# Kernel optimization log

Measured on AMD Instinct MI355X. Metric: run time of the kernel, lower is better.

## Reference

```python
import jax, jax.numpy as jnp
import numpy as np
from jax import lax

B, T, E, H = 16, 1024, 512, 1024


def setup_inputs() -> dict:
    key = jax.random.key(0)
    ks = jax.random.split(key, 10)
    s = 0.1
    return {
        "x":   jax.random.normal(ks[0], (B, T, E), jnp.float32),
        # reset gate: sigmoid(x@Wxr + h@Whr + br)
        "Wxr": jax.random.normal(ks[1], (E, H), jnp.float32) * s,
        "Whr": jax.random.normal(ks[2], (H, H), jnp.float32) * s,
        "br":  jax.random.normal(ks[3], (H,), jnp.float32) * s,
        # update gate: sigmoid(x@Wxz + h@Whz + bz)
        "Wxz": jax.random.normal(ks[4], (E, H), jnp.float32) * s,
        "Whz": jax.random.normal(ks[5], (H, H), jnp.float32) * s,
        "bz":  jax.random.normal(ks[6], (H,), jnp.float32) * s,
        # candidate: tanh(r * (h@Wh) + x@Wi + b)
        "Wi":  jax.random.normal(ks[7], (E, H), jnp.float32) * s,
        "Wh":  jax.random.normal(ks[8], (H, H), jnp.float32) * s,
        "b":   jax.random.normal(ks[9], (H,), jnp.float32) * s,
    }


def reference(x, Wxr, Whr, br, Wxz, Whz, bz, Wi, Wh, b):
    # Batch all input-to-hidden projections across time up front.
    xr = jnp.einsum("bte,eh->bth", x, Wxr) + br  # [B,T,H]
    xz = jnp.einsum("bte,eh->bth", x, Wxz) + bz
    xi = jnp.einsum("bte,eh->bth", x, Wi) + b

    def step(h, inp):
        xr_t, xz_t, xi_t = inp  # each [B,H]
        r = jax.nn.sigmoid(xr_t + h @ Whr)
        z = jax.nn.sigmoid(xz_t + h @ Whz)
        cand = jnp.tanh(r * (h @ Wh) + xi_t)
        h_new = z * h + (1.0 - z) * cand
        return h_new, h_new

    h0 = jnp.zeros((x.shape[0], Wh.shape[0]), x.dtype)
    # scan over time: move T to leading axis
    _, hs = lax.scan(step, h0, (xr.transpose(1, 0, 2), xz.transpose(1, 0, 2), xi.transpose(1, 0, 2)))
    return hs.transpose(1, 0, 2)  # [B,T,H]
```

## Files before the change

kernel.cpp:

```cpp
#include <hip/hip_runtime.h>
#include <hip/hip_bf16.h>
#include <cstddef>
#include <cstdint>

static constexpr int BB = 16;
static constexpr int TT = 1024;
static constexpr int EE = 512;
static constexpr int HH = 1024;

static constexpr int NG   = 4;
static constexpr int GBLK = 64;
static constexpr int BPG  = 4;
static constexpr int COLS = 16;

using u32 = unsigned int;
typedef float f32x4 __attribute__((ext_vector_type(4)));

static constexpr u32 PZ = 0x7FC0DEADu;

__device__ __forceinline__ float st_load(const float* p) { return *p; }
__device__ __forceinline__ float st_load(const __hip_bfloat16* p) { return __bfloat162float(*p); }
__device__ __forceinline__ void st_store(float* p, float v) { *p = v; }
__device__ __forceinline__ void st_store(__hip_bfloat16* p, float v) { *p = __float2bfloat16(v); }

__device__ __forceinline__ void llc_load(f32x4& d, const f32x4* p) {
    asm volatile("global_load_dwordx4 %0, %1, off sc0 sc1" : "=v"(d) : "v"(p));
}
__device__ __forceinline__ void llc_drain() {
    asm volatile("s_waitcnt vmcnt(0)" ::: "memory");
    __builtin_amdgcn_sched_barrier(0);
}
__device__ __forceinline__ bool ok4(const f32x4 v) {
    return __float_as_uint(v[0]) != PZ && __float_as_uint(v[1]) != PZ &&
           __float_as_uint(v[2]) != PZ && __float_as_uint(v[3]) != PZ;
}

#define FMA4(ACC, S, W)                         \
    (ACC).x = fmaf((S), (W).x, (ACC).x);        \
    (ACC).y = fmaf((S), (W).y, (ACC).y);        \
    (ACC).z = fmaf((S), (W).z, (ACC).z);        \
    (ACC).w = fmaf((S), (W).w, (ACC).w);

template <typename ST>
__global__ __launch_bounds__(256) void proj_kernel(
    const float* __restrict__ x,
    const float* __restrict__ Wxr, const float* __restrict__ br,
    const float* __restrict__ Wxz, const float* __restrict__ bz,
    const float* __restrict__ Wi,  const float* __restrict__ bi,
    ST* __restrict__ xr_out, ST* __restrict__ xz_out, float* __restrict__ xi_out,
    u32* __restrict__ bar)
{
    __shared__ float xT[16][68];
    __shared__ float wB[3][16][64];

    const int tid = threadIdx.x;
    if (blockIdx.x == 0 && blockIdx.y == 0) bar[tid] = 0u;

    const int tx = tid & 15, ty = tid >> 4;
    const int m0 = blockIdx.y * 64, n0 = blockIdx.x * 64;
    const float* Wg[3] = {Wxr, Wxz, Wi};

    float4 acc[3][4];
#pragma unroll
    for (int g = 0; g < 3; ++g)
#pragma unroll
        for (int i = 0; i < 4; ++i) acc[g][i] = make_float4(0.f, 0.f, 0.f, 0.f);

    const int xrow = tid >> 2, xk = (tid & 3) * 4;
    const int wk = tid >> 4, wn = (tid & 15) * 4;

    for (int k0 = 0; k0 < EE; k0 += 16) {
        float4 xv = *(const float4*)(x + (size_t)(m0 + xrow) * EE + k0 + xk);
        xT[xk + 0][xrow] = xv.x;
        xT[xk + 1][xrow] = xv.y;
        xT[xk + 2][xrow] = xv.z;
        xT[xk + 3][xrow] = xv.w;
#pragma unroll
        for (int g = 0; g < 3; ++g) {
            float4 wv = *(const float4*)(Wg[g] + (size_t)(k0 + wk) * HH + n0 + wn);
            *(float4*)&wB[g][wk][wn] = wv;
        }
        __syncthreads();
#pragma unroll
        for (int kk = 0; kk < 16; ++kk) {
            float4 a  = *(const float4*)&xT[kk][ty * 4];
            float4 w0 = *(const float4*)&wB[0][kk][tx * 4];
            float4 w1 = *(const float4*)&wB[1][kk][tx * 4];
            float4 w2 = *(const float4*)&wB[2][kk][tx * 4];
            float as[4] = {a.x, a.y, a.z, a.w};
#pragma unroll
            for (int i = 0; i < 4; ++i) {
                FMA4(acc[0][i], as[i], w0);
                FMA4(acc[1][i], as[i], w1);
                FMA4(acc[2][i], as[i], w2);
            }
        }
        __syncthreads();
    }

    float4 bv0 = *(const float4*)(br + n0 + tx * 4);
    float4 bv1 = *(const float4*)(bz + n0 + tx * 4);
    float4 bv2 = *(const float4*)(bi + n0 + tx * 4);
#pragma unroll
    for (int i = 0; i < 4; ++i) {
        size_t m = (size_t)m0 + ty * 4 + i;
        size_t off = m * HH + n0 + tx * 4;
        float4 v0 = acc[0][i]; v0.x += bv0.x; v0.y += bv0.y; v0.z += bv0.z; v0.w += bv0.w;
        float4 v1 = acc[1][i]; v1.x += bv1.x; v1.y += bv1.y; v1.z += bv1.z; v1.w += bv1.w;
        float4 v2 = acc[2][i]; v2.x += bv2.x; v2.y += bv2.y; v2.z += bv2.z; v2.w += bv2.w;
        st_store(xr_out + off + 0, v0.x); st_store(xr_out + off + 1, v0.y);
        st_store(xr_out + off + 2, v0.z); st_store(xr_out + off + 3, v0.w);
        st_store(xz_out + off + 0, v1.x); st_store(xz_out + off + 1, v1.y);
        st_store(xz_out + off + 2, v1.z); st_store(xz_out + off + 3, v1.w);
        *(float4*)(xi_out + off) = v2;
    }
}

__device__ __forceinline__ float row16_allreduce(float v) {
    int y;
    y = __builtin_amdgcn_update_dpp(0, __float_as_int(v), 0xB1, 0xF, 0xF, true);
    v += __int_as_float(y);
    y = __builtin_amdgcn_update_dpp(0, __float_as_int(v), 0x4E, 0xF, 0xF, true);
    v += __int_as_float(y);
    y = __builtin_amdgcn_update_dpp(0, __float_as_int(v), 0x124, 0xF, 0xF, true);
    v += __int_as_float(y);
    y = __builtin_amdgcn_update_dpp(0, __float_as_int(v), 0x128, 0xF, 0xF, true);
    v += __int_as_float(y);
    return v;
}

__device__ __forceinline__ void xbar(u32* ctr, unsigned target) {
    __syncthreads();
    if (threadIdx.x == 0) {
        asm volatile("s_waitcnt vmcnt(0)" ::: "memory");
        __builtin_amdgcn_sched_barrier(0);
        __hip_atomic_fetch_add(ctr, 1u, __ATOMIC_RELAXED, __HIP_MEMORY_SCOPE_AGENT);
        while (__hip_atomic_load(ctr, __ATOMIC_RELAXED, __HIP_MEMORY_SCOPE_AGENT) < target) {
            __builtin_amdgcn_s_sleep(1);
        }
        __builtin_amdgcn_sched_barrier(0);
    }
    __syncthreads();
}

template <typename ST>
__global__ __launch_bounds__(512, 1) void scan_kernel(
    const ST* __restrict__ xr, const ST* __restrict__ xz,
    const float* __restrict__ Whr, const float* __restrict__ Whz, const float* __restrict__ Wh,
    float* __restrict__ out,
    float* __restrict__ hbuf,
    u32* __restrict__ bar)
{
    __shared__ f32x4 hsx[8][4][32];
    __shared__ float red[8][4][48];
    __shared__ float pre[48][4];

    const int tid = threadIdx.x, bid = blockIdx.x;
    const int lane = tid & 63, wv = tid >> 6;
    const int cgg = lane >> 4, kslo = lane & 15;
    const int ks = wv * 16 + kslo;
    const int group = bid >> 6, gb = bid & 63;
    const int n0 = gb * COLS;
    u32* ctr = bar + group * 64;

    float wreg[12][8];
    {
        const float* WG[3] = {Whr, Whz, Wh};
#pragma unroll
        for (int u = 0; u < 12; ++u) {
            int ugc = cgg * 12 + u;
            const float* W = WG[ugc >> 4];
            int col = n0 + (ugc & 15);
#pragma unroll
            for (int j = 0; j < 8; ++j)
                wreg[u][j] = W[(size_t)(ks * 8 + j) * HH + col];
        }
    }

    const float pzf = __uint_as_float(PZ);
    const int tb4 = tid >> 4, tc = tid & 15;
    const int tbg = group * BPG + tb4;
    const int coln = n0 + tc;

    float pxr = 0.f, pxz = 0.f, pxi = 0.f, hprev = 0.f;
    if (tid < 64) {
        float* b0 = hbuf + group * (BPG * HH) + tb4 * HH + coln;
        __hip_atomic_store(b0,         0.f, __ATOMIC_RELAXED, __HIP_MEMORY_SCOPE_AGENT);
        __hip_atomic_store(b0 + 16384, pzf, __ATOMIC_RELAXED, __HIP_MEMORY_SCOPE_AGENT);
        __hip_atomic_store(b0 + 32768, pzf, __ATOMIC_RELAXED, __HIP_MEMORY_SCOPE_AGENT);
        __hip_atomic_store(b0 + 49152, pzf, __ATOMIC_RELAXED, __HIP_MEMORY_SCOPE_AGENT);
        size_t idx0 = (size_t)(tbg * TT) * HH + coln;
        pxr = st_load(xr + idx0); pxz = st_load(xz + idx0); pxi = out[idx0];
    }
    xbar(ctr, GBLK);

    const int b_ld = lane >> 4;
    const int s_rot = (((lane & 15) + (gb & 15)) * 2) & 31;

    for (int t = 0; t < TT; ++t) {
        {
            const f32x4* p = (const f32x4*)hbuf + (size_t)(t & 3) * 4096
                             + group * 1024 + b_ld * 256 + wv * 32 + s_rot;
            f32x4 va, vb;
            for (;;) {
                llc_load(va, p); llc_load(vb, p + 1); llc_drain();
                if (ok4(va) && ok4(vb)) break;
                __builtin_amdgcn_s_sleep(1);
            }
            hsx[wv][b_ld][s_rot]     = va;
            hsx[wv][b_ld][s_rot + 1] = vb;
            asm volatile("s_waitcnt lgkmcnt(0)" ::: "memory");
            __builtin_amdgcn_sched_barrier(0);
        }

        if (tid < 64 && t + 2 < TT) {
            __hip_atomic_store(hbuf + (size_t)((t + 2) & 3) * 16384
                               + group * (BPG * HH) + tb4 * HH + coln,
                               pzf, __ATOMIC_RELAXED, __HIP_MEMORY_SCOPE_AGENT);
        }

        float pacc[4][12];
#pragma unroll
        for (int b = 0; b < 4; ++b)
#pragma unroll
            for (int u = 0; u < 12; ++u) pacc[b][u] = 0.f;

#pragma unroll
        for (int b = 0; b < 4; ++b) {
            f32x4 ha = hsx[wv][b][2 * kslo];
            f32x4 hb = hsx[wv][b][2 * kslo + 1];
#pragma unroll
            for (int u = 0; u < 12; ++u) {
                float a = pacc[b][u];
                a = fmaf(ha[0], wreg[u][0], a);
                a = fmaf(ha[1], wreg[u][1], a);
                a = fmaf(ha[2], wreg[u][2], a);
                a = fmaf(ha[3], wreg[u][3], a);
                a = fmaf(hb[0], wreg[u][4], a);
                a = fmaf(hb[1], wreg[u][5], a);
                a = fmaf(hb[2], wreg[u][6], a);
                a = fmaf(hb[3], wreg[u][7], a);
                pacc[b][u] = a;
            }
        }

#pragma unroll
        for (int b = 0; b < 4; ++b)
#pragma unroll
            for (int u = 0; u < 12; ++u) pacc[b][u] = row16_allreduce(pacc[b][u]);

        if (kslo == 0) {
#pragma unroll
            for (int b = 0; b < 4; ++b)
#pragma unroll
                for (int u = 0; u < 12; ++u) red[wv][cgg][b * 12 + u] = pacc[b][u];
        }
        __syncthreads();

        if (tid < 192) {
            int b4 = tid & 3, ugc = tid >> 2;
            int cq = ugc / 12, u = ugc - cq * 12;
            float s = 0.f;
#pragma unroll
            for (int w = 0; w < 8; ++w) s += red[w][cq][b4 * 12 + u];
            pre[ugc][b4] = s;
        }
        __syncthreads();

        if (tid < 64) {
            float dr = pre[tc][tb4], dz = pre[16 + tc][tb4], dh = pre[32 + tc][tb4];
            float r = 1.f / (1.f + expf(-(dr + pxr)));
            float z = 1.f / (1.f + expf(-(dz + pxz)));
            float cand = tanhf(fmaf(r, dh, pxi));
            float hnew = fmaf(z, hprev - cand, cand);
            hprev = hnew;
            asm volatile("s_waitcnt vmcnt(0)" ::: "memory");
            __builtin_amdgcn_sched_barrier(0);
            if (t + 1 < TT) {
                __hip_atomic_store(hbuf + (size_t)((t + 1) & 3) * 16384
                                   + group * (BPG * HH) + tb4 * HH + coln,
                                   hnew, __ATOMIC_RELAXED, __HIP_MEMORY_SCOPE_AGENT);
            }
            size_t idx = (size_t)(tbg * TT + t) * HH + coln;
            out[idx] = hnew;
            if (t + 1 < TT) {
                size_t idx2 = idx + HH;
                pxr = st_load(xr + idx2); pxz = st_load(xz + idx2); pxi = out[idx2];
            }
        }
    }
}

__global__ void sentinel_kernel(float* out) {
    if (threadIdx.x == 0 && blockIdx.x == 0) out[0] = 12345.0f;
}

extern "C" void kernel_launch(void* const* d_in, const int* in_sizes, int n_in,
                              void* d_out, int out_size, void* d_ws, size_t ws_size,
                              hipStream_t stream) {
    const float* x   = (const float*)d_in[0];
    const float* Wxr = (const float*)d_in[1];
    const float* Whr = (const float*)d_in[2];
    const float* br  = (const float*)d_in[3];
    const float* Wxz = (const float*)d_in[4];
    const float* Whz = (const float*)d_in[5];
    const float* bz  = (const float*)d_in[6];
    const float* Wi  = (const float*)d_in[7];
    const float* Wh  = (const float*)d_in[8];
    const float* bb  = (const float*)d_in[9];
    float* out = (float*)d_out;

    const size_t BTH = (size_t)BB * TT * HH;
    const size_t HBUF_ELTS = (size_t)4 * BB * HH;
    const size_t BAR_BYTES = 4096;
    const size_t need_f32 = 2 * BTH * sizeof(float) + HBUF_ELTS * sizeof(float) + BAR_BYTES;
    const size_t need_b16 = 2 * BTH * sizeof(__hip_bfloat16) + HBUF_ELTS * sizeof(float) + BAR_BYTES;

    dim3 pgrid(HH / 64, (BB * TT) / 64);

    if (ws_size >= need_f32) {
        float* xr = (float*)d_ws;
        float* xz = xr + BTH;
        float* hb = xz + BTH;
        u32* bar = (u32*)(hb + HBUF_ELTS);
        proj_kernel<float><<<pgrid, 256, 0, stream>>>(x, Wxr, br, Wxz, bz, Wi, bb, xr, xz, out, bar);
        const float* xrc = xr; const float* xzc = xz;
        void* args[8] = {(void*)&xrc, (void*)&xzc, (void*)&Whr, (void*)&Whz,
                         (void*)&Wh, (void*)&out, (void*)&hb, (void*)&bar};
        hipLaunchCooperativeKernel((void*)scan_kernel<float>, dim3(256), dim3(512),
                                   args, 0, stream);
    } else if (ws_size >= need_b16) {
        __hip_bfloat16* xr = (__hip_bfloat16*)d_ws;
        __hip_bfloat16* xz = xr + BTH;
        float* hb = (float*)(xz + BTH);
        u32* bar = (u32*)(hb + HBUF_ELTS);
        proj_kernel<__hip_bfloat16><<<pgrid, 256, 0, stream>>>(x, Wxr, br, Wxz, bz, Wi, bb, xr, xz, out, bar);
        const __hip_bfloat16* xrc = xr; const __hip_bfloat16* xzc = xz;
        void* args[8] = {(void*)&xrc, (void*)&xzc, (void*)&Whr, (void*)&Whz,
                         (void*)&Wh, (void*)&out, (void*)&hb, (void*)&bar};
        hipLaunchCooperativeKernel((void*)scan_kernel<__hip_bfloat16>, dim3(256), dim3(512),
                                   args, 0, stream);
    } else {
        sentinel_kernel<<<1, 64, 0, stream>>>(out);
    }
}
```

Measured before the change: 5.192 ms.

## Repartition GRU scan into eight smaller groups with 1024-thread blocks

The recurrent scan is split into 8 groups of 32 blocks, each handling 2 batch rows and 32 hidden columns, instead of 4 groups of 64 blocks handling 4 rows and 16 columns. Each block now runs 16 waves, split into two halves over the gate columns, and 8 K-slices per half. Each thread polls one f32x4 of the hidden state instead of two. The intent is to shrink the per-step cross-block barrier and hidden-state exchange to fewer participants and spread per-step work across more waves. The cost is higher register pressure: each thread still holds 96 weight registers, and `__launch_bounds__(1024, 4)` may force spills. Occupancy constraints for the cooperative launch also change.

```diff
diff --git a/kernel.cpp b/kernel.cpp
--- a/kernel.cpp
+++ b/kernel.cpp
@@ -8,10 +8,10 @@
 static constexpr int EE = 512;
 static constexpr int HH = 1024;
 
-static constexpr int NG   = 4;
-static constexpr int GBLK = 64;
-static constexpr int BPG  = 4;
-static constexpr int COLS = 16;
+static constexpr int NG   = 8;
+static constexpr int GBLK = 32;
+static constexpr int BPG  = 2;
+static constexpr int COLS = 32;
 
 using u32 = unsigned int;
 typedef float f32x4 __attribute__((ext_vector_type(4)));
@@ -144,47 +144,47 @@
 }
 
 template <typename ST>
-__global__ __launch_bounds__(512, 1) void scan_kernel(
+__global__ __launch_bounds__(1024, 4) void scan_kernel(
     const ST* __restrict__ xr, const ST* __restrict__ xz,
     const float* __restrict__ Whr, const float* __restrict__ Whz, const float* __restrict__ Wh,
     float* __restrict__ out,
     float* __restrict__ hbuf,
     u32* __restrict__ bar)
 {
-    __shared__ f32x4 hsx[8][4][32];
-    __shared__ float red[8][4][48];
-    __shared__ float pre[48][4];
+    __shared__ f32x4 hsx[16][BPG][32];
+    __shared__ float red[16][4][24];
+    __shared__ float pre[96][BPG];
 
     const int tid = threadIdx.x, bid = blockIdx.x;
     const int lane = tid & 63, wv = tid >> 6;
     const int cgg = lane >> 4, kslo = lane & 15;
-    const int ks = wv * 16 + kslo;
-    const int group = bid >> 6, gb = bid & 63;
+    const int wu = wv >> 3, wk = wv & 7;
+    const int group = bid >> 5, gb = bid & 31;
     const int n0 = gb * COLS;
-    u32* ctr = bar + group * 64;
+    u32* ctr = bar + group * 32;
 
     float wreg[12][8];
     {
         const float* WG[3] = {Whr, Whz, Wh};
 #pragma unroll
         for (int u = 0; u < 12; ++u) {
-            int ugc = cgg * 12 + u;
-            const float* W = WG[ugc >> 4];
-            int col = n0 + (ugc & 15);
+            int ugc = wu * 48 + cgg * 12 + u;
+            const float* W = WG[ugc >> 5];
+            int col = n0 + (ugc & 31);
 #pragma unroll
             for (int j = 0; j < 8; ++j)
-                wreg[u][j] = W[(size_t)(ks * 8 + j) * HH + col];
+                wreg[u][j] = W[(size_t)(wk * 128 + kslo * 8 + j) * HH + col];
         }
     }
 
     const float pzf = __uint_as_float(PZ);
-    const int tb4 = tid >> 4, tc = tid & 15;
-    const int tbg = group * BPG + tb4;
+    const int tb2 = tid >> 5, tc = tid & 31;
+    const int tbg = group * BPG + tb2;
     const int coln = n0 + tc;
 
     float pxr = 0.f, pxz = 0.f, pxi = 0.f, hprev = 0.f;
     if (tid < 64) {
-        float* b0 = hbuf + group * (BPG * HH) + tb4 * HH + coln;
+        float* b0 = hbuf + group * (BPG * HH) + tb2 * HH + coln;
         __hip_atomic_store(b0,         0.f, __ATOMIC_RELAXED, __HIP_MEMORY_SCOPE_AGENT);
         __hip_atomic_store(b0 + 16384, pzf, __ATOMIC_RELAXED, __HIP_MEMORY_SCOPE_AGENT);
         __hip_atomic_store(b0 + 32768, pzf, __ATOMIC_RELAXED, __HIP_MEMORY_SCOPE_AGENT);
@@ -194,39 +194,38 @@
     }
     xbar(ctr, GBLK);
 
-    const int b_ld = lane >> 4;
-    const int s_rot = (((lane & 15) + (gb & 15)) * 2) & 31;
+    const int b_ld = lane >> 5;
+    const int s_rot = ((lane & 31) + gb) & 31;
+    const int g_base = group * (BPG * 256) + b_ld * 256 + wk * 32 + s_rot;
 
     for (int t = 0; t < TT; ++t) {
         {
-            const f32x4* p = (const f32x4*)hbuf + (size_t)(t & 3) * 4096
-                             + group * 1024 + b_ld * 256 + wv * 32 + s_rot;
-            f32x4 va, vb;
+            const f32x4* p = (const f32x4*)hbuf + (size_t)(t & 3) * 4096 + g_base;
+            f32x4 va;
             for (;;) {
-                llc_load(va, p); llc_load(vb, p + 1); llc_drain();
-                if (ok4(va) && ok4(vb)) break;
+                llc_load(va, p); llc_drain();
+                if (ok4(va)) break;
                 __builtin_amdgcn_s_sleep(1);
             }
-            hsx[wv][b_ld][s_rot]     = va;
-            hsx[wv][b_ld][s_rot + 1] = vb;
+            hsx[wv][b_ld][s_rot] = va;
             asm volatile("s_waitcnt lgkmcnt(0)" ::: "memory");
             __builtin_amdgcn_sched_barrier(0);
         }
 
         if (tid < 64 && t + 2 < TT) {
             __hip_atomic_store(hbuf + (size_t)((t + 2) & 3) * 16384
-                               + group * (BPG * HH) + tb4 * HH + coln,
+                               + group * (BPG * HH) + tb2 * HH + coln,
                                pzf, __ATOMIC_RELAXED, __HIP_MEMORY_SCOPE_AGENT);
         }
 
-        float pacc[4][12];
-#pragma unroll
-        for (int b = 0; b < 4; ++b)
+        float pacc[BPG][12];
+#pragma unroll
+        for (int b = 0; b < BPG; ++b)
 #pragma unroll
             for (int u = 0; u < 12; ++u) pacc[b][u] = 0.f;
 
 #pragma unroll
-        for (int b = 0; b < 4; ++b) {
+        for (int b = 0; b < BPG; ++b) {
             f32x4 ha = hsx[wv][b][2 * kslo];
             f32x4 hb = hsx[wv][b][2 * kslo + 1];
 #pragma unroll
@@ -245,30 +244,32 @@
         }
 
 #pragma unroll
-        for (int b = 0; b < 4; ++b)
+        for (int b = 0; b < BPG; ++b)
 #pragma unroll
             for (int u = 0; u < 12; ++u) pacc[b][u] = row16_allreduce(pacc[b][u]);
 
         if (kslo == 0) {
 #pragma unroll
-            for (int b = 0; b < 4; ++b)
+            for (int b = 0; b < BPG; ++b)
 #pragma unroll
                 for (int u = 0; u < 12; ++u) red[wv][cgg][b * 12 + u] = pacc[b][u];
         }
         __syncthreads();
 
         if (tid < 192) {
-            int b4 = tid & 3, ugc = tid >> 2;
-            int cq = ugc / 12, u = ugc - cq * 12;
+            int b2 = tid & 1, ugc = tid >> 1;
+            int uh = (ugc >= 48);
+            int ug = ugc - uh * 48;
+            int cq = ug / 12, u = ug - cq * 12;
             float s = 0.f;
 #pragma unroll
-            for (int w = 0; w < 8; ++w) s += red[w][cq][b4 * 12 + u];
-            pre[ugc][b4] = s;
+            for (int w = 0; w < 8; ++w) s += red[uh * 8 + w][cq][b2 * 12 + u];
+            pre[ugc][b2] = s;
         }
         __syncthreads();
 
         if (tid < 64) {
-            float dr = pre[tc][tb4], dz = pre[16 + tc][tb4], dh = pre[32 + tc][tb4];
+            float dr = pre[tc][tb2], dz = pre[32 + tc][tb2], dh = pre[64 + tc][tb2];
             float r = 1.f / (1.f + expf(-(dr + pxr)));
             float z = 1.f / (1.f + expf(-(dz + pxz)));
             float cand = tanhf(fmaf(r, dh, pxi));
@@ -278,7 +279,7 @@
             __builtin_amdgcn_sched_barrier(0);
             if (t + 1 < TT) {
                 __hip_atomic_store(hbuf + (size_t)((t + 1) & 3) * 16384
-                                   + group * (BPG * HH) + tb4 * HH + coln,
+                                   + group * (BPG * HH) + tb2 * HH + coln,
                                    hnew, __ATOMIC_RELAXED, __HIP_MEMORY_SCOPE_AGENT);
             }
             size_t idx = (size_t)(tbg * TT + t) * HH + coln;
@@ -317,6 +318,7 @@
     const size_t need_b16 = 2 * BTH * sizeof(__hip_bfloat16) + HBUF_ELTS * sizeof(float) + BAR_BYTES;
 
     dim3 pgrid(HH / 64, (BB * TT) / 64);
+    dim3 sgrid(NG * GBLK);
 
     if (ws_size >= need_f32) {
         float* xr = (float*)d_ws;
@@ -327,7 +329,7 @@
         const float* xrc = xr; const float* xzc = xz;
         void* args[8] = {(void*)&xrc, (void*)&xzc, (void*)&Whr, (void*)&Whz,
                          (void*)&Wh, (void*)&out, (void*)&hb, (void*)&bar};
-        hipLaunchCooperativeKernel((void*)scan_kernel<float>, dim3(256), dim3(512),
+        hipLaunchCooperativeKernel((void*)scan_kernel<float>, sgrid, dim3(1024),
                                    args, 0, stream);
     } else if (ws_size >= need_b16) {
         __hip_bfloat16* xr = (__hip_bfloat16*)d_ws;
@@ -338,7 +340,7 @@
         const __hip_bfloat16* xrc = xr; const __hip_bfloat16* xzc = xz;
         void* args[8] = {(void*)&xrc, (void*)&xzc, (void*)&Whr, (void*)&Whz,
                          (void*)&Wh, (void*)&out, (void*)&hb, (void*)&bar};
-        hipLaunchCooperativeKernel((void*)scan_kernel<__hip_bfloat16>, dim3(256), dim3(512),
+        hipLaunchCooperativeKernel((void*)scan_kernel<__hip_bfloat16>, sgrid, dim3(1024),
                                    args, 0, stream);
     } else {
         sentinel_kernel<<<1, 64, 0, stream>>>(out);
```

Result: slower. 14.30 ms (+175.4%).
